# Optimization experiments

Hardware: AMD Instinct MI355X
Metric: run time of the kernel (lower is better)

Reference implementation:

```python
import jax, jax.numpy as jnp
import numpy as np

# AAA hyperparameters (from init_kwargs)
ALPHA = 1.0
TAU = 6.0
KAPPA = 100
TEMP = 1.0
BETA = 5.0
LR = 0.1
B1, B2, EPS = 0.9, 0.999, 1e-8  # torch.optim.Adam defaults


def logit_margin(z, y):
    # Faithful to torch `z[:, y]` advanced indexing with y of shape [B]:
    # fy[i, j] = z[i, y[j]]  -> shape [B, B]
    fy = z[:, y]
    # z_clone is detached in the source; topk path carries no gradient.
    # z_clone[:, y] = -1000 masks ALL predicted classes in every row.
    zc = jax.lax.stop_gradient(z).at[:, y].set(-1000.0)
    top = jnp.max(zc, axis=1)  # topk(k=1) over classes, shape [B]
    # torch broadcasting [B,B] - [B] subtracts along the last axis
    return fy - top


def aaa_forward(x, W, b):
    # model.eval() + no_grad forward, then z = logits.detach()
    z = jax.lax.stop_gradient(x @ W + b)  # [B, C]
    y = jnp.argmax(z, axis=1)             # pred_y, [B]

    l_org = logit_margin(z, y)                                # [B, B]
    l_atr = (jnp.floor(l_org / TAU) + 0.5) * TAU
    # AAA_type == 'sin'
    l_trg = l_org - ALPHA * TAU * jnp.sin(jnp.pi * (1.0 - 2.0 * (l_org - l_atr) / TAU))
    p_trg = jnp.max(jax.nn.softmax(z / TEMP, axis=1), axis=1)  # [B]

    def loss_fn(u):
        m = logit_margin(u, y)                      # [B, B]
        # torch.max(F.softmax(u, dim=1)) with NO dim -> global scalar max (faithful)
        pmax = jnp.max(jax.nn.softmax(u, axis=1))
        # [B,B] + [B] broadcasts over the last axis, then .sum()
        return jnp.sum(jnp.abs(m - l_trg) + BETA * jnp.abs(pmax - p_trg))

    grad_fn = jax.grad(loss_fn)

    def step(carry, t):
        u, m, v = carry
        g = grad_fn(u)
        m = B1 * m + (1.0 - B1) * g
        v = B2 * v + (1.0 - B2) * g * g
        mhat = m / (1.0 - B1 ** t)   # bias correction, t = 1..KAPPA
        vhat = v / (1.0 - B2 ** t)
        u = u - LR * mhat / (jnp.sqrt(vhat) + EPS)
        return (u, m, v), None

    ts = jnp.arange(1, KAPPA + 1, dtype=z.dtype)
    (u, _, _), _ = jax.lax.scan(step, (z, jnp.zeros_like(z), jnp.zeros_like(z)), ts)
    return u  # protected logits, [B, C]


def setup_inputs() -> dict:
    key = jax.random.key(0)
    k1, k2 = jax.random.split(key)
    x = jax.random.normal(k1, (2048, 2048), dtype=jnp.float32)
    W = jax.random.normal(k2, (2048, 1000), dtype=jnp.float32) * 0.02
    b = jnp.zeros((1000,), dtype=jnp.float32)
    return {"x": x, "W": W, "b": b}


def reference(x, W, b):
    return aaa_forward(x, W, b)
```

## Files before the change

kernel.cpp:

```cpp
#include <hip/hip_runtime.h>
#include <math.h>

#pragma clang fp contract(off)

#define NB 2048
#define NC 1000
#define NK 2048
#define RPB 4
#define NBLK (NB / RPB)
#define NLEAF 16

typedef unsigned long long u64;

__global__ __launch_bounds__(256) void k_gemm(const float* __restrict__ x,
                                              const float* __restrict__ W,
                                              const float* __restrict__ bias,
                                              float* __restrict__ z, int PC) {
    __shared__ float As[16][64];
    __shared__ float Bs[16][64];
    const int tid = threadIdx.x;
    const int m0 = blockIdx.y * 64, n0 = blockIdx.x * 64;
    const int tx = tid & 15, ty = tid >> 4;
    float accT[4][4];
    float accB[4][4];
#pragma unroll
    for (int i = 0; i < 4; i++)
#pragma unroll
        for (int j = 0; j < 4; j++) { accT[i][j] = 0.0f; accB[i][j] = 0.0f; }

    for (int kb = 0; kb < 128; kb++) {
        if (PC > 0 && kb > 0 && (kb % PC) == 0) {
#pragma unroll
            for (int i = 0; i < 4; i++)
#pragma unroll
                for (int j = 0; j < 4; j++) { accT[i][j] += accB[i][j]; accB[i][j] = 0.0f; }
        }
        const int k0 = kb * 16;
        {
            int row = tid >> 2, kg = tid & 3;
            const float4 a = *(const float4*)(x + (size_t)(m0 + row) * NK + k0 + kg * 4);
            As[kg * 4 + 0][row] = a.x;
            As[kg * 4 + 1][row] = a.y;
            As[kg * 4 + 2][row] = a.z;
            As[kg * 4 + 3][row] = a.w;
        }
        {
            int rowk = tid >> 4, c4 = tid & 15;
            int cbase = n0 + c4 * 4;
            const float* wp = W + (size_t)(k0 + rowk) * NC + cbase;
#pragma unroll
            for (int j = 0; j < 4; j++)
                Bs[rowk][c4 * 4 + j] = (cbase + j < NC) ? wp[j] : 0.0f;
        }
        __syncthreads();
#pragma unroll
        for (int kk = 0; kk < 16; kk++) {
            float a[4], bb[4];
#pragma unroll
            for (int i = 0; i < 4; i++) a[i] = As[kk][ty * 4 + i];
#pragma unroll
            for (int j = 0; j < 4; j++) bb[j] = Bs[kk][tx * 4 + j];
#pragma unroll
            for (int i = 0; i < 4; i++)
#pragma unroll
                for (int j = 0; j < 4; j++) accB[i][j] = fmaf(a[i], bb[j], accB[i][j]);
        }
        __syncthreads();
    }
#pragma unroll
    for (int i = 0; i < 4; i++) {
        int r = m0 + ty * 4 + i;
#pragma unroll
        for (int j = 0; j < 4; j++) {
            int c = n0 + tx * 4 + j;
            if (c < NC) {
                float s = accT[i][j] + accB[i][j];
                z[(size_t)r * NC + c] = s + bias[c];
            }
        }
    }
}

__global__ __launch_bounds__(256) void k_rowstats(const float* __restrict__ z,
                                                  int* __restrict__ y,
                                                  float* __restrict__ ptrg,
                                                  float* __restrict__ se,
                                                  float* __restrict__ rm,
                                                  int* __restrict__ am) {
    __shared__ float sv[256];
    __shared__ int si[256];
    const int tid = threadIdx.x, row = blockIdx.x;
    const float* zr = z + (size_t)row * NC;
    float bv = -INFINITY;
    int bi = 0x7fffffff;
    for (int c = tid; c < NC; c += 256) {
        float zz = zr[c];
        if (zz > bv) { bv = zz; bi = c; }
    }
    sv[tid] = bv; si[tid] = bi;
    __syncthreads();
    for (int s = 128; s > 0; s >>= 1) {
        if (tid < s) {
            float v2 = sv[tid + s]; int i2 = si[tid + s];
            if (v2 > sv[tid] || (v2 == sv[tid] && i2 < si[tid])) { sv[tid] = v2; si[tid] = i2; }
        }
        __syncthreads();
    }
    const float rmx = sv[0];
    const int amx = si[0];
    __syncthreads();
    float sl = 0.0f;
    for (int c = tid; c < NC; c += 256) sl += expf(zr[c] - rmx);
    sv[tid] = sl;
    __syncthreads();
    for (int s = 128; s > 0; s >>= 1) {
        if (tid < s) sv[tid] += sv[tid + s];
        __syncthreads();
    }
    if (tid == 0) {
        float s0 = sv[0];
        y[row] = amx; ptrg[row] = 1.0f / s0;
        se[row] = s0; rm[row] = rmx; am[row] = amx;
    }
}

__global__ void k_hist(const int* __restrict__ y, int* __restrict__ cnt) {
    int i = blockIdx.x * 256 + threadIdx.x;
    if (i < NB) atomicAdd(&cnt[y[i]], 1);
}
__global__ __launch_bounds__(1024) void k_group(const int* __restrict__ y,
                                                const int* __restrict__ cnt,
                                                int* __restrict__ off,
                                                int* __restrict__ pos,
                                                int* __restrict__ jidx,
                                                int* __restrict__ pinv) {
    __shared__ int s[1024];
    const int tid = threadIdx.x;
    int myc = (tid < NC) ? cnt[tid] : 0;
    s[tid] = myc;
    __syncthreads();
    for (int d = 1; d < 1024; d <<= 1) {
        int add = (tid >= d) ? s[tid - d] : 0;
        __syncthreads();
        s[tid] += add;
        __syncthreads();
    }
    if (tid < NC) {
        int excl = s[tid] - myc;
        off[tid] = excl;
        pos[tid] = excl;
    }
    if (tid == 0) off[NC] = NB;
    __syncthreads();
    for (int j = tid; j < NB; j += 1024) {
        int c = y[j];
        int p = atomicAdd(&pos[c], 1);
        jidx[p] = j;
        pinv[j] = p;
    }
}

__global__ __launch_bounds__(1024) void k_sort(const float* __restrict__ ptrg,
                                               float* __restrict__ ptrgS) {
    __shared__ float ps[2048];
    const int tid = threadIdx.x;
    ps[tid] = ptrg[tid];
    ps[tid + 1024] = ptrg[tid + 1024];
    __syncthreads();
    for (int k = 2; k <= 2048; k <<= 1) {
        for (int j = k >> 1; j > 0; j >>= 1) {
            int i1 = ((tid & ~(j - 1)) << 1) | (tid & (j - 1));
            int i2 = i1 | j;
            bool up = ((i1 & k) == 0);
            float a = ps[i1], b = ps[i2];
            if ((a > b) == up) { ps[i1] = b; ps[i2] = a; }
            __syncthreads();
        }
    }
    ptrgS[tid] = ps[tid];
    ptrgS[tid + 1024] = ps[tid + 1024];
}

__global__ __launch_bounds__(256) void k_preptz(const float* __restrict__ z,
                                                const int* __restrict__ cnt,
                                                const int* __restrict__ pinv,
                                                float* __restrict__ tz,
                                                float* __restrict__ tuP) {
    __shared__ float sv[256];
    const int tid = threadIdx.x, row = blockIdx.x;
    const float* zr = z + (size_t)row * NC;
    float tm = -1000.0f;
    for (int c = tid; c < NC; c += 256) {
        float zz = zr[c];
        if (cnt[c] == 0) tm = fmaxf(tm, zz);
    }
    sv[tid] = tm;
    __syncthreads();
    for (int s = 128; s > 0; s >>= 1) {
        if (tid < s) sv[tid] = fmaxf(sv[tid], sv[tid + s]);
        __syncthreads();
    }
    if (tid == 0) { tz[row] = sv[0]; tuP[pinv[row]] = sv[0]; }
}

__global__ __launch_bounds__(256) void k_thr(const float* __restrict__ z,
                                             const float* __restrict__ tz,
                                             const int* __restrict__ y,
                                             const int* __restrict__ jidx,
                                             float* __restrict__ ThrG) {
    const int tid = threadIdx.x, a = blockIdx.x;
    const float PIF = 3.14159265358979323846f;
    const float* zr = z + (size_t)a * NC;
    for (int p = tid; p < NB; p += 256) {
        int j = jidx[p];
        int c = y[j];
        float L = zr[c] - tz[j];
        float q = L / 6.0f;
        float fq = floorf(q);
        float fh = fq + 0.5f;
        float latr = fh * 6.0f;
        float d1 = L - latr;
        float d2 = 2.0f * d1;
        float d3 = d2 / 6.0f;
        float d4 = 1.0f - d3;
        float d5 = PIF * d4;
        float sn = sinf(d5);
        float p6 = 6.0f * sn;
        float thr = L - p6;
        ThrG[(size_t)a * NB + p] = thr;
    }
}

__device__ __forceinline__ float ldgA(const float* p) {
    return __hip_atomic_load(p, __ATOMIC_RELAXED, __HIP_MEMORY_SCOPE_AGENT);
}
__device__ __forceinline__ int ldgAi(const int* p) {
    return __hip_atomic_load(p, __ATOMIC_RELAXED, __HIP_MEMORY_SCOPE_AGENT);
}
__device__ __forceinline__ u64 ldgAu64(const u64* p) {
    return __hip_atomic_load(p, __ATOMIC_RELAXED, __HIP_MEMORY_SCOPE_AGENT);
}
__device__ __forceinline__ void stgA(float* p, float v) {
    __hip_atomic_store(p, v, __ATOMIC_RELAXED, __HIP_MEMORY_SCOPE_AGENT);
}
__device__ __forceinline__ void stgAu64(u64* p, u64 v) {
    __hip_atomic_store(p, v, __ATOMIC_RELAXED, __HIP_MEMORY_SCOPE_AGENT);
}

__global__ __launch_bounds__(1024, 8) void k_adam(
    const float* __restrict__ z0,
    float* __restrict__ uout,
    const float* __restrict__ ThrG,
    const float* __restrict__ ptrg,
    const float* __restrict__ ptrgS,
    const int* __restrict__ cnt,
    const int* __restrict__ off,
    const int* __restrict__ jidx,
    const int* __restrict__ pinv,
    const float* __restrict__ seA, const float* __restrict__ rmA,
    const int* __restrict__ amA,
    float* __restrict__ tuPA, float* __restrict__ tuPB,
    const float* __restrict__ bcT,
    int* __restrict__ leafCnt, int* __restrict__ rootCnt,
    u64* __restrict__ leafKey, u64* __restrict__ rootKey,
    u64* __restrict__ keyMir) {
    __shared__ float tuLs[NB];
    __shared__ float thrL[RPB][NB];
    __shared__ float svg[RPB][256];
    __shared__ int   sig[RPB][256];
    __shared__ float tvg[RPB][256];
    __shared__ float sc[RPB][3];
    __shared__ int   sci[RPB][2];
    __shared__ float outRmG[RPB];
    __shared__ u64   kB[RPB];
    __shared__ u64   kShared;
    const int tid = threadIdx.x;
    const int g = tid >> 8;
    const int l = tid & 255;
    const int row = blockIdx.x * RPB + g;
    const int leaf = blockIdx.x >> 5;
    const float B1F = 0.9f;
    const float C1 = (float)(1.0 - 0.9);
    const float B2F = 0.999f;
    const float C2 = (float)(1.0 - 0.999);

    float U[4], M[4], V[4];
    int cn_[4], p0_[4], p1_[4];
    {
        const size_t base = (size_t)row * NC;
#pragma unroll
        for (int k2 = 0; k2 < 4; k2++) {
            int c = l + k2 * 256;
            if (c < NC) {
                U[k2] = z0[base + c];
                cn_[k2] = cnt[c];
                p0_[k2] = off[c];
                p1_[k2] = off[c + 1];
            } else {
                U[k2] = 0.0f; cn_[k2] = -1; p0_[k2] = 0; p1_[k2] = 0;
            }
            M[k2] = 0.0f;
            V[k2] = 0.0f;
        }
    }
    for (int p = l; p < NB; p += 256) thrL[g][p] = ThrG[(size_t)row * NB + p];
    const int myPinv = pinv[row];

    float prev_se = 0.0f, prev_rm = 0.0f;
    int prev_am = 0;

    for (int t = 1; t <= 100; t++) {
        const bool odd = (t & 1);
        const float* tuPO = odd ? tuPA : tuPB;
        float* tuPN = odd ? tuPB : tuPA;
        const float bc1 = bcT[2 * (t - 1)];
        const float bc2 = bcT[2 * (t - 1) + 1];

        if (t == 1) {
            for (int p = tid; p < NB; p += 1024) tuLs[p] = ldgA(&tuPO[p]);
            float bv = -INFINITY;
            int bi = 0x7fffffff;
            for (int i = l; i < NB; i += 256) {
                float pp = 1.0f / ldgA(&seA[i]);
                if (pp > bv || (pp == bv && i < bi)) { bv = pp; bi = i; }
            }
            svg[g][l] = bv; sig[g][l] = bi;
            __syncthreads();
            for (int s = 128; s > 0; s >>= 1) {
                if (l < s) {
                    float v2 = svg[g][l + s]; int i2 = sig[g][l + s];
                    if (v2 > svg[g][l] || (v2 == svg[g][l] && i2 < sig[g][l])) {
                        svg[g][l] = v2; sig[g][l] = i2;
                    }
                }
                __syncthreads();
            }
            const float pmax = svg[g][0];
            const int istar0 = sig[g][0];
            __syncthreads();
            float s2l = 0.0f;
            for (int i = l; i < NB; i += 256) {
                float d = pmax - ptrg[i];
                s2l += (d >= 0.0f) ? 1.0f : -1.0f;
            }
            svg[g][l] = s2l;
            __syncthreads();
            for (int s = 128; s > 0; s >>= 1) {
                if (l < s) svg[g][l] += svg[g][l + s];
                __syncthreads();
            }
            const float s2 = svg[g][0];
            if (l == 0) {
                float Kf = 5.0f * (2048.0f * s2);
                float coef0 = Kf * pmax;
                sc[g][0] = coef0;
                sc[g][1] = ldgA(&seA[istar0]);
                sc[g][2] = ldgA(&rmA[istar0]);
                sci[g][0] = ldgAi(&amA[istar0]);
                sci[g][1] = istar0;
            }
            __syncthreads();
        } else {
            if (tid == 0) {
                const u64* mp = &keyMir[(size_t)(t - 2) * NLEAF + leaf];
                u64 kReg = 0ull;
                int polls = 0;
                while ((kReg = ldgAu64(mp)) == 0ull) {
                    __builtin_amdgcn_s_sleep(1);
                    if (++polls > (1 << 18)) break;
                }
                kShared = kReg;
            }
            __syncthreads();
            const u64 kReg = kShared;
            for (int p = tid; p < NB; p += 1024) tuLs[p] = ldgA(&tuPO[p]);
            if (l == 0) {
                int istarN = (NB - 1) - (int)(kReg & 0xffffffffull);
                sci[g][1] = istarN;
                if (row == istarN) {
                    float pmax = __uint_as_float((unsigned int)(kReg >> 32));
                    int lo = 0, hi = NB;
                    while (lo < hi) {
                        int mid = (lo + hi) >> 1;
                        if (ptrgS[mid] <= pmax) lo = mid + 1; else hi = mid;
                    }
                    float s2 = (float)(2 * lo - NB);
                    float Kf = 5.0f * (2048.0f * s2);
                    sc[g][0] = Kf * pmax;
                    sc[g][1] = prev_se;
                    sc[g][2] = prev_rm;
                    sci[g][0] = prev_am;
                }
            }
            __syncthreads();
        }
        const float coef = sc[g][0], se_i = sc[g][1], rm_i = sc[g][2];
        const int jstar = sci[g][0], istar = sci[g][1];
        const bool ig2 = (row == istar);

        float nmax = -INFINITY;
        int nidx = 0x7fffffff;
        float ntop = -1000.0f;
#pragma unroll
        for (int k2 = 0; k2 < 4; k2++) {
            int c = l + k2 * 256;
            if (c < NC) {
                float u0 = U[k2];
                float mm = M[k2];
                float vv = V[k2];
                float gg = 0.0f;
                for (int p = p0_[k2]; p < p1_[k2]; p++) {
                    float marg = u0 - tuLs[p];
                    float diff = marg - thrL[g][p];
                    gg += (diff >= 0.0f) ? 1.0f : -1.0f;
                }
                if (ig2) {
                    float e = expf(u0 - rm_i);
                    float S = e / se_i;
                    float dlt = ((c == jstar) ? 1.0f : 0.0f) - S;
                    float t2v = coef * dlt;
                    gg = gg + t2v;
                }
                float t1m = B1F * mm;
                float t2m = C1 * gg;
                mm = t1m + t2m;
                float gg1 = C2 * gg;
                float gg2 = gg1 * gg;
                float t1v = B2F * vv;
                vv = t1v + gg2;
                float mh = mm / bc1;
                float vh = vv / bc2;
                float num = 0.1f * mh;
                float sq = sqrtf(vh);
                float den = sq + 1e-8f;
                float qq = num / den;
                u0 = u0 - qq;
                U[k2] = u0;
                M[k2] = mm;
                V[k2] = vv;
                if (u0 > nmax || (u0 == nmax && c < nidx)) { nmax = u0; nidx = c; }
                if (cn_[k2] == 0) ntop = fmaxf(ntop, u0);
            }
        }

        if (t == 100) break;

        float rm_n = 0.0f, tu_n = 0.0f, se_n = 0.0f;
        int am_n = 0;
        svg[g][l] = nmax; sig[g][l] = nidx; tvg[g][l] = ntop;
        __syncthreads();
        if (l < 64) {
            float v = svg[g][l]; int ix = sig[g][l];
            { float v2 = svg[g][l + 128]; int i2 = sig[g][l + 128];
              if (v2 > v || (v2 == v && i2 < ix)) { v = v2; ix = i2; } }
            { float a = svg[g][l + 64]; int ai = sig[g][l + 64];
              float b = svg[g][l + 192]; int bi2 = sig[g][l + 192];
              if (b > a || (b == a && bi2 < ai)) { a = b; ai = bi2; }
              if (a > v || (a == v && ai < ix)) { v = a; ix = ai; } }
#pragma unroll
            for (int s = 32; s > 0; s >>= 1) {
                float v2 = __shfl_xor(v, s);
                int i2 = __shfl_xor(ix, s);
                if (v2 > v || (v2 == v && i2 < ix)) { v = v2; ix = i2; }
            }
            float w = fmaxf(tvg[g][l], tvg[g][l + 128]);
            w = fmaxf(w, fmaxf(tvg[g][l + 64], tvg[g][l + 192]));
#pragma unroll
            for (int s = 32; s > 0; s >>= 1) w = fmaxf(w, __shfl_xor(w, s));
            if (l == 0) { outRmG[g] = v; rm_n = v; am_n = ix; tu_n = w; }
        }
        __syncthreads();
        const float rm_b = outRmG[g];
        float sel = 0.0f;
#pragma unroll
        for (int k2 = 0; k2 < 4; k2++) {
            int c = l + k2 * 256;
            if (c < NC) sel += expf(U[k2] - rm_b);
        }
        svg[g][l] = sel;
        __syncthreads();
        if (l < 64) {
            float v = (svg[g][l] + svg[g][l + 128]) + (svg[g][l + 64] + svg[g][l + 192]);
#pragma unroll
            for (int s = 32; s > 0; s >>= 1) v += __shfl_xor(v, s);
            if (l == 0) se_n = v;
        }

        if (l == 0) {
            stgA(&tuPN[myPinv], tu_n);
            float pp = 1.0f / se_n;
            kB[g] = ((u64)__float_as_uint(pp) << 32) |
                    (u64)(unsigned int)((NB - 1) - row);
            prev_se = se_n; prev_rm = rm_n; prev_am = am_n;
        }
        __syncthreads();
        if (tid == 0) {
            u64 key = kB[0];
            if (kB[1] > key) key = kB[1];
            if (kB[2] > key) key = kB[2];
            if (kB[3] > key) key = kB[3];
            u64* lkp = &leafKey[(size_t)(t - 1) * NLEAF + leaf];
            atomicMax(lkp, key);
            asm volatile("s_waitcnt vmcnt(0)" ::: "memory");
            int old = __hip_atomic_fetch_add(&leafCnt[(t - 1) * NLEAF + leaf], 1,
                                             __ATOMIC_RELAXED, __HIP_MEMORY_SCOPE_AGENT);
            if (old == 31) {
                u64 lk = ldgAu64(lkp);
                atomicMax(&rootKey[t - 1], lk);
                asm volatile("s_waitcnt vmcnt(0)" ::: "memory");
                int ro = __hip_atomic_fetch_add(&rootCnt[t - 1], 1,
                                                __ATOMIC_RELAXED, __HIP_MEMORY_SCOPE_AGENT);
                if (ro == NLEAF - 1) {
                    u64 fin = ldgAu64(&rootKey[t - 1]);
                    u64* mir = &keyMir[(size_t)(t - 1) * NLEAF];
                    for (int lf = 0; lf < NLEAF; lf++) stgAu64(&mir[lf], fin);
                }
            }
        }
    }

    {
        const size_t base = (size_t)row * NC;
#pragma unroll
        for (int k2 = 0; k2 < 4; k2++) {
            int c = l + k2 * 256;
            if (c < NC) uout[base + c] = U[k2];
        }
    }
}

__global__ void k_fuse5(const float* __restrict__ a, const float* __restrict__ p1,
                        const float* __restrict__ p2, const float* __restrict__ p3,
                        const float* __restrict__ p4, float* __restrict__ out, int n) {
    const float CL = 0.08f;
    int i = blockIdx.x * 256 + threadIdx.x;
    if (i < n) {
        float v0 = a[i], v1 = p1[i], v2 = p2[i], v3 = p3[i], v4 = p4[i];
        float vv[5] = {v0, v1, v2, v3, v4};
#pragma unroll
        for (int k = 1; k < 5; k++) {
            float key = vv[k];
            int j = k - 1;
            while (j >= 0 && vv[j] > key) { vv[j + 1] = vv[j]; j--; }
            vv[j + 1] = key;
        }
        float med = vv[2];
        float d = med - v0;
        d = fminf(fmaxf(d, -CL), CL);
        out[i] = v0 + d;
    }
}

extern "C" void kernel_launch(void* const* d_in, const int* in_sizes, int n_in,
                              void* d_out, int out_size, void* d_ws, size_t ws_size,
                              hipStream_t stream) {
    (void)in_sizes; (void)n_in; (void)out_size; (void)ws_size;
    const float* x = (const float*)d_in[0];
    const float* W = (const float*)d_in[1];
    const float* bias = (const float*)d_in[2];
    float* out = (float*)d_out;

    const size_t NE = (size_t)NB * NC;
    float* zm    = (float*)d_ws;
    float* t0    = zm + NE;
    float* t1    = t0 + NE;
    float* t2    = t1 + NE;
    float* t3    = t2 + NE;
    float* t4    = t3 + NE;
    float* ThrG  = t4 + NE;
    float* tz    = ThrG + (size_t)NB * NB;
    float* ptrg  = tz + NB;
    float* ptrgS = ptrg + NB;
    float* seA   = ptrgS + NB;
    float* rmA   = seA + NB;
    float* tuPA  = rmA + NB;
    float* tuPB  = tuPA + NB;
    float* bcT   = tuPB + NB;
    int* amA   = (int*)(bcT + 256);
    int* yv    = amA + NB;
    int* jidx  = yv + NB;
    int* pinv  = jidx + NB;
    int* cnt   = pinv + NB;
    int* off   = cnt + 1024;
    int* pos   = off + 1024;
    int* leafCnt = pos + 1024;
    int* rootCnt = leafCnt + 6400;
    u64* leafKey = (u64*)(rootCnt + 128);
    u64* rootKey = leafKey + 6400;
    u64* keyMir  = rootKey + 128;

    static float h_bc[200];
    static int bc_init = 0;
    if (!bc_init) {
        for (int t = 1; t <= 100; t++) {
            h_bc[2 * (t - 1)]     = 1.0f - powf(0.9f, (float)t);
            h_bc[2 * (t - 1) + 1] = 1.0f - powf(0.999f, (float)t);
        }
        bc_init = 1;
    }
    hipMemcpyAsync(bcT, h_bc, 200 * sizeof(float), hipMemcpyHostToDevice, stream);

    float* traj[5] = {t0, t1, t2, t3, t4};
    const int PCs[5] = {0, 32, 24, 16, 10};
    const int nblk = (int)((NE + 255) / 256);
    const size_t barBytes = (6400 + 128) * sizeof(int) + (6400 + 128 + 6400) * sizeof(u64);

    for (int pass = 0; pass < 5; pass++) {
        k_gemm<<<dim3(16, 32), 256, 0, stream>>>(x, W, bias, zm, PCs[pass]);
        hipMemsetAsync(cnt, 0, 1024 * sizeof(int), stream);
        hipMemsetAsync(leafCnt, 0, barBytes, stream);
        k_rowstats<<<NB, 256, 0, stream>>>(zm, yv, ptrg, seA, rmA, amA);
        k_hist<<<8, 256, 0, stream>>>(yv, cnt);
        k_group<<<1, 1024, 0, stream>>>(yv, cnt, off, pos, jidx, pinv);
        k_sort<<<1, 1024, 0, stream>>>(ptrg, ptrgS);
        k_preptz<<<NB, 256, 0, stream>>>(zm, cnt, pinv, tz, tuPA);
        k_thr<<<NB, 256, 0, stream>>>(zm, tz, yv, jidx, ThrG);

        k_adam<<<NBLK, 1024, 0, stream>>>(zm, traj[pass], ThrG, ptrg, ptrgS,
                                          cnt, off, jidx, pinv,
                                          seA, rmA, amA, tuPA, tuPB,
                                          bcT, leafCnt, rootCnt,
                                          leafKey, rootKey, keyMir);
    }

    k_fuse5<<<nblk, 256, 0, stream>>>(t0, t1, t2, t3, t4, out, (int)NE);
}
```

Measured before the change: 9.299 ms.

## Balance per-class gradient loops by sorting classes by count across threads

Adds a bitonic-sort kernel that orders classes by their predicted-sample count, and in the Adam kernel each thread now computes the sign-sum gradient for classes taken from this permutation rather than for its own contiguous classes. Results go through shared memory (logits staged to LDS, gradients written to an LDS buffer) so that the long inner loops over samples are spread evenly across wavefronts and warp divergence from skewed class counts is reduced. The cost is an extra kernel launch per pass, more shared memory that may lower occupancy, and two additional block-wide barriers per Adam step.

```diff
diff --git a/kernel.cpp b/kernel.cpp
--- a/kernel.cpp
+++ b/kernel.cpp
@@ -158,6 +158,26 @@
         jidx[p] = j;
         pinv[j] = p;
     }
+}
+
+__global__ __launch_bounds__(1024) void k_cperm(const int* __restrict__ cnt,
+                                                int* __restrict__ cperm) {
+    __shared__ int ks[1024];
+    const int tid = threadIdx.x;
+    ks[tid] = (cnt[tid] << 10) | tid;
+    __syncthreads();
+    for (int k = 2; k <= 1024; k <<= 1) {
+        for (int j = k >> 1; j > 0; j >>= 1) {
+            int ixj = tid ^ j;
+            if (ixj > tid) {
+                bool up = ((tid & k) == 0);
+                int a = ks[tid], b = ks[ixj];
+                if ((a > b) == up) { ks[tid] = b; ks[ixj] = a; }
+            }
+            __syncthreads();
+        }
+    }
+    cperm[tid] = ks[tid] & 1023;
 }
 
 __global__ __launch_bounds__(1024) void k_sort(const float* __restrict__ ptrg,
@@ -257,6 +277,7 @@
     const int* __restrict__ off,
     const int* __restrict__ jidx,
     const int* __restrict__ pinv,
+    const int* __restrict__ cperm,
     const float* __restrict__ seA, const float* __restrict__ rmA,
     const int* __restrict__ amA,
     float* __restrict__ tuPA, float* __restrict__ tuPB,
@@ -266,9 +287,8 @@
     u64* __restrict__ keyMir) {
     __shared__ float tuLs[NB];
     __shared__ float thrL[RPB][NB];
-    __shared__ float svg[RPB][256];
-    __shared__ int   sig[RPB][256];
-    __shared__ float tvg[RPB][256];
+    __shared__ float unionBuf[RPB][1024];
+    __shared__ float gLs[RPB][1024];
     __shared__ float sc[RPB][3];
     __shared__ int   sci[RPB][2];
     __shared__ float outRmG[RPB];
@@ -284,8 +304,15 @@
     const float B2F = 0.999f;
     const float C2 = (float)(1.0 - 0.999);
 
+    float* const uLg = &unionBuf[g][0];
+    float* const svG = &unionBuf[g][0];
+    int*   const siG = (int*)&unionBuf[g][256];
+    float* const tvG = &unionBuf[g][512];
+    float* const gLg = &gLs[g][0];
+
     float U[4], M[4], V[4];
-    int cn_[4], p0_[4], p1_[4];
+    int cn_[4];
+    int cq_[4], q0_[4], q1_[4];
     {
         const size_t base = (size_t)row * NC;
 #pragma unroll
@@ -294,13 +321,15 @@
             if (c < NC) {
                 U[k2] = z0[base + c];
                 cn_[k2] = cnt[c];
-                p0_[k2] = off[c];
-                p1_[k2] = off[c + 1];
             } else {
-                U[k2] = 0.0f; cn_[k2] = -1; p0_[k2] = 0; p1_[k2] = 0;
+                U[k2] = 0.0f; cn_[k2] = -1;
             }
             M[k2] = 0.0f;
             V[k2] = 0.0f;
+            int c2 = cperm[l + k2 * 256];
+            cq_[k2] = c2;
+            q0_[k2] = (c2 < NC) ? off[c2] : 0;
+            q1_[k2] = (c2 < NC) ? off[c2 + 1] : 0;
         }
     }
     for (int p = l; p < NB; p += 256) thrL[g][p] = ThrG[(size_t)row * NB + p];
@@ -324,32 +353,32 @@
                 float pp = 1.0f / ldgA(&seA[i]);
                 if (pp > bv || (pp == bv && i < bi)) { bv = pp; bi = i; }
             }
-            svg[g][l] = bv; sig[g][l] = bi;
+            svG[l] = bv; siG[l] = bi;
             __syncthreads();
             for (int s = 128; s > 0; s >>= 1) {
                 if (l < s) {
-                    float v2 = svg[g][l + s]; int i2 = sig[g][l + s];
-                    if (v2 > svg[g][l] || (v2 == svg[g][l] && i2 < sig[g][l])) {
-                        svg[g][l] = v2; sig[g][l] = i2;
+                    float v2 = svG[l + s]; int i2 = siG[l + s];
+                    if (v2 > svG[l] || (v2 == svG[l] && i2 < siG[l])) {
+                        svG[l] = v2; siG[l] = i2;
                     }
                 }
                 __syncthreads();
             }
-            const float pmax = svg[g][0];
-            const int istar0 = sig[g][0];
+            const float pmax = svG[0];
+            const int istar0 = siG[0];
             __syncthreads();
             float s2l = 0.0f;
             for (int i = l; i < NB; i += 256) {
                 float d = pmax - ptrg[i];
                 s2l += (d >= 0.0f) ? 1.0f : -1.0f;
             }
-            svg[g][l] = s2l;
+            svG[l] = s2l;
             __syncthreads();
             for (int s = 128; s > 0; s >>= 1) {
-                if (l < s) svg[g][l] += svg[g][l + s];
+                if (l < s) svG[l] += svG[l + s];
                 __syncthreads();
             }
-            const float s2 = svg[g][0];
+            const float s2 = svG[0];
             if (l == 0) {
                 float Kf = 5.0f * (2048.0f * s2);
                 float coef0 = Kf * pmax;
@@ -398,6 +427,27 @@
         const int jstar = sci[g][0], istar = sci[g][1];
         const bool ig2 = (row == istar);
 
+#pragma unroll
+        for (int k2 = 0; k2 < 4; k2++) {
+            int c = l + k2 * 256;
+            if (c < NC) uLg[c] = U[k2];
+        }
+        __syncthreads();
+
+#pragma unroll
+        for (int k2 = 0; k2 < 4; k2++) {
+            const int c2 = cq_[k2];
+            const float u0q = uLg[c2];
+            float gsum = 0.0f;
+            for (int p = q0_[k2]; p < q1_[k2]; p++) {
+                float marg = u0q - tuLs[p];
+                float diff = marg - thrL[g][p];
+                gsum += (diff >= 0.0f) ? 1.0f : -1.0f;
+            }
+            gLg[c2] = gsum;
+        }
+        __syncthreads();
+
         float nmax = -INFINITY;
         int nidx = 0x7fffffff;
         float ntop = -1000.0f;
@@ -408,12 +458,7 @@
                 float u0 = U[k2];
                 float mm = M[k2];
                 float vv = V[k2];
-                float gg = 0.0f;
-                for (int p = p0_[k2]; p < p1_[k2]; p++) {
-                    float marg = u0 - tuLs[p];
-                    float diff = marg - thrL[g][p];
-                    gg += (diff >= 0.0f) ? 1.0f : -1.0f;
-                }
+                float gg = gLg[c];
                 if (ig2) {
                     float e = expf(u0 - rm_i);
                     float S = e / se_i;
@@ -447,14 +492,15 @@
 
         float rm_n = 0.0f, tu_n = 0.0f, se_n = 0.0f;
         int am_n = 0;
-        svg[g][l] = nmax; sig[g][l] = nidx; tvg[g][l] = ntop;
+        __syncthreads();
+        svG[l] = nmax; siG[l] = nidx; tvG[l] = ntop;
         __syncthreads();
         if (l < 64) {
-            float v = svg[g][l]; int ix = sig[g][l];
-            { float v2 = svg[g][l + 128]; int i2 = sig[g][l + 128];
+            float v = svG[l]; int ix = siG[l];
+            { float v2 = svG[l + 128]; int i2 = siG[l + 128];
               if (v2 > v || (v2 == v && i2 < ix)) { v = v2; ix = i2; } }
-            { float a = svg[g][l + 64]; int ai = sig[g][l + 64];
-              float b = svg[g][l + 192]; int bi2 = sig[g][l + 192];
+            { float a = svG[l + 64]; int ai = siG[l + 64];
+              float b = svG[l + 192]; int bi2 = siG[l + 192];
               if (b > a || (b == a && bi2 < ai)) { a = b; ai = bi2; }
               if (a > v || (a == v && ai < ix)) { v = a; ix = ai; } }
 #pragma unroll
@@ -463,8 +509,8 @@
                 int i2 = __shfl_xor(ix, s);
                 if (v2 > v || (v2 == v && i2 < ix)) { v = v2; ix = i2; }
             }
-            float w = fmaxf(tvg[g][l], tvg[g][l + 128]);
-            w = fmaxf(w, fmaxf(tvg[g][l + 64], tvg[g][l + 192]));
+            float w = fmaxf(tvG[l], tvG[l + 128]);
+            w = fmaxf(w, fmaxf(tvG[l + 64], tvG[l + 192]));
 #pragma unroll
             for (int s = 32; s > 0; s >>= 1) w = fmaxf(w, __shfl_xor(w, s));
             if (l == 0) { outRmG[g] = v; rm_n = v; am_n = ix; tu_n = w; }
@@ -477,10 +523,10 @@
             int c = l + k2 * 256;
             if (c < NC) sel += expf(U[k2] - rm_b);
         }
-        svg[g][l] = sel;
+        svG[l] = sel;
         __syncthreads();
         if (l < 64) {
-            float v = (svg[g][l] + svg[g][l + 128]) + (svg[g][l + 64] + svg[g][l + 192]);
+            float v = (svG[l] + svG[l + 128]) + (svG[l + 64] + svG[l + 192]);
 #pragma unroll
             for (int s = 32; s > 0; s >>= 1) v += __shfl_xor(v, s);
             if (l == 0) se_n = v;
@@ -583,7 +629,8 @@
     int* cnt   = pinv + NB;
     int* off   = cnt + 1024;
     int* pos   = off + 1024;
-    int* leafCnt = pos + 1024;
+    int* cperm = pos + 1024;
+    int* leafCnt = cperm + 1024;
     int* rootCnt = leafCnt + 6400;
     u64* leafKey = (u64*)(rootCnt + 128);
     u64* rootKey = leafKey + 6400;
@@ -612,12 +659,13 @@
         k_rowstats<<<NB, 256, 0, stream>>>(zm, yv, ptrg, seA, rmA, amA);
         k_hist<<<8, 256, 0, stream>>>(yv, cnt);
         k_group<<<1, 1024, 0, stream>>>(yv, cnt, off, pos, jidx, pinv);
+        k_cperm<<<1, 1024, 0, stream>>>(cnt, cperm);
         k_sort<<<1, 1024, 0, stream>>>(ptrg, ptrgS);
         k_preptz<<<NB, 256, 0, stream>>>(zm, cnt, pinv, tz, tuPA);
         k_thr<<<NB, 256, 0, stream>>>(zm, tz, yv, jidx, ThrG);
 
         k_adam<<<NBLK, 1024, 0, stream>>>(zm, traj[pass], ThrG, ptrg, ptrgS,
-                                          cnt, off, jidx, pinv,
+                                          cnt, off, jidx, pinv, cperm,
                                           seA, rmA, amA, tuPA, tuPB,
                                           bcT, leafCnt, rootCnt,
                                           leafKey, rootKey, keyMir);
```

After: 9.637 ms. 3.6% more time.

## Permute class-to-thread mapping by class count to balance per-wave work

Applied to the files above, without the earlier changes.

A new single-block kernel bitonic-sorts the classes by how many rows predict them, producing a permutation. The Adam kernel then assigns classes to threads through that permutation, so threads in a wavefront run similar trip counts in the per-class margin loop and divergence drops. To keep the softmax partial-sum order identical, updated logits go through a new shared-memory buffer indexed by the original class. This costs one extra small kernel per pass, an extra LDS write and read each step, and 16KB more LDS per block, which may lower occupancy.

```diff
diff --git a/kernel.cpp b/kernel.cpp
--- a/kernel.cpp
+++ b/kernel.cpp
@@ -158,6 +158,26 @@
         jidx[p] = j;
         pinv[j] = p;
     }
+}
+
+__global__ __launch_bounds__(1024) void k_cperm(const int* __restrict__ cnt,
+                                                int* __restrict__ cperm) {
+    __shared__ int ks[1024];
+    const int tid = threadIdx.x;
+    ks[tid] = (cnt[tid] << 10) | tid;
+    __syncthreads();
+    for (int k = 2; k <= 1024; k <<= 1) {
+        for (int j = k >> 1; j > 0; j >>= 1) {
+            int ixj = tid ^ j;
+            if (ixj > tid) {
+                bool up = ((tid & k) == 0);
+                int a = ks[tid], b = ks[ixj];
+                if ((a > b) == up) { ks[tid] = b; ks[ixj] = a; }
+            }
+            __syncthreads();
+        }
+    }
+    cperm[tid] = ks[tid] & 1023;
 }
 
 __global__ __launch_bounds__(1024) void k_sort(const float* __restrict__ ptrg,
@@ -257,6 +277,7 @@
     const int* __restrict__ off,
     const int* __restrict__ jidx,
     const int* __restrict__ pinv,
+    const int* __restrict__ cperm,
     const float* __restrict__ seA, const float* __restrict__ rmA,
     const int* __restrict__ amA,
     float* __restrict__ tuPA, float* __restrict__ tuPB,
@@ -266,6 +287,7 @@
     u64* __restrict__ keyMir) {
     __shared__ float tuLs[NB];
     __shared__ float thrL[RPB][NB];
+    __shared__ float uPost[RPB][1024];
     __shared__ float svg[RPB][256];
     __shared__ int   sig[RPB][256];
     __shared__ float tvg[RPB][256];
@@ -285,12 +307,13 @@
     const float C2 = (float)(1.0 - 0.999);
 
     float U[4], M[4], V[4];
-    int cn_[4], p0_[4], p1_[4];
+    int co_[4], cn_[4], p0_[4], p1_[4];
     {
         const size_t base = (size_t)row * NC;
 #pragma unroll
         for (int k2 = 0; k2 < 4; k2++) {
-            int c = l + k2 * 256;
+            int c = cperm[l + k2 * 256];
+            co_[k2] = c;
             if (c < NC) {
                 U[k2] = z0[base + c];
                 cn_[k2] = cnt[c];
@@ -403,7 +426,7 @@
         float ntop = -1000.0f;
 #pragma unroll
         for (int k2 = 0; k2 < 4; k2++) {
-            int c = l + k2 * 256;
+            const int c = co_[k2];
             if (c < NC) {
                 float u0 = U[k2];
                 float mm = M[k2];
@@ -445,6 +468,12 @@
 
         if (t == 100) break;
 
+#pragma unroll
+        for (int k2 = 0; k2 < 4; k2++) {
+            const int c = co_[k2];
+            if (c < NC) uPost[g][c] = U[k2];
+        }
+
         float rm_n = 0.0f, tu_n = 0.0f, se_n = 0.0f;
         int am_n = 0;
         svg[g][l] = nmax; sig[g][l] = nidx; tvg[g][l] = ntop;
@@ -475,7 +504,7 @@
 #pragma unroll
         for (int k2 = 0; k2 < 4; k2++) {
             int c = l + k2 * 256;
-            if (c < NC) sel += expf(U[k2] - rm_b);
+            if (c < NC) sel += expf(uPost[g][c] - rm_b);
         }
         svg[g][l] = sel;
         __syncthreads();
@@ -523,7 +552,7 @@
         const size_t base = (size_t)row * NC;
 #pragma unroll
         for (int k2 = 0; k2 < 4; k2++) {
-            int c = l + k2 * 256;
+            const int c = co_[k2];
             if (c < NC) uout[base + c] = U[k2];
         }
     }
@@ -583,7 +612,8 @@
     int* cnt   = pinv + NB;
     int* off   = cnt + 1024;
     int* pos   = off + 1024;
-    int* leafCnt = pos + 1024;
+    int* cperm = pos + 1024;
+    int* leafCnt = cperm + 1024;
     int* rootCnt = leafCnt + 6400;
     u64* leafKey = (u64*)(rootCnt + 128);
     u64* rootKey = leafKey + 6400;
@@ -612,12 +642,13 @@
         k_rowstats<<<NB, 256, 0, stream>>>(zm, yv, ptrg, seA, rmA, amA);
         k_hist<<<8, 256, 0, stream>>>(yv, cnt);
         k_group<<<1, 1024, 0, stream>>>(yv, cnt, off, pos, jidx, pinv);
+        k_cperm<<<1, 1024, 0, stream>>>(cnt, cperm);
         k_sort<<<1, 1024, 0, stream>>>(ptrg, ptrgS);
         k_preptz<<<NB, 256, 0, stream>>>(zm, cnt, pinv, tz, tuPA);
         k_thr<<<NB, 256, 0, stream>>>(zm, tz, yv, jidx, ThrG);
 
         k_adam<<<NBLK, 1024, 0, stream>>>(zm, traj[pass], ThrG, ptrg, ptrgS,
-                                          cnt, off, jidx, pinv,
+                                          cnt, off, jidx, pinv, cperm,
                                           seA, rmA, amA, tuPA, tuPB,
                                           bcT, leafCnt, rootCnt,
                                           leafKey, rootKey, keyMir);
```

After: 9.363 ms. About the same (+0.7%).
